# Optimization experiments

Measured on AMD Instinct MI355X. Metric: run time of the kernel, lower is better.

## Reference

```python
import jax, jax.numpy as jnp
import numpy as np

C1 = 0.01 ** 2
C2 = 0.03 ** 2
IN_CH = 3
WIN = 11
LEVELS = 5


def _gauss_kernel(k=WIN, sigma=1.5, c=IN_CH):
    ax = np.arange(k, dtype=np.float32) - (k - 1) / 2.0
    g = np.exp(-(ax ** 2) / (2.0 * sigma ** 2))
    g = g / g.sum()
    w2d = np.outer(g, g).astype(np.float32)  # [k,k]
    return jnp.asarray(np.tile(w2d[None, None], (c, 1, 1, 1)))  # [C,1,k,k]


def _dwconv(x, w):
    # depthwise (grouped) conv, 'same' padding for odd kernel
    pad = (w.shape[-1] - 1) // 2
    return jax.lax.conv_general_dilated(
        x, w, window_strides=(1, 1), padding=[(pad, pad), (pad, pad)],
        feature_group_count=x.shape[1],
        dimension_numbers=("NCHW", "OIHW", "NCHW"))


def _ssim_loss(i1, i2, w):
    m1 = _dwconv(i1, w)
    m2 = _dwconv(i2, w)
    m1sq = m1 * m1
    m2sq = m2 * m2
    m12 = m1 * m2
    s1 = _dwconv(i1 * i1, w) - m1sq
    s2 = _dwconv(i2 * i2, w) - m2sq
    s12 = _dwconv(i1 * i2, w) - m12
    ssim = (2 * m12 + C1) * (2 * s12 + C2) / ((m1sq + m2sq + C1) * (s1 + s2 + C2))
    return 1.0 - ssim.mean()


def _avg_pool2(x):
    B, C, H, W = x.shape
    return x.reshape(B, C, H // 2, 2, W // 2, 2).mean(axis=(3, 5))


def setup_inputs() -> dict:
    key = jax.random.key(0)
    k1, k2 = jax.random.split(key)
    img1 = jax.random.uniform(k1, (16, IN_CH, 512, 512), dtype=jnp.float32)
    img2 = jax.random.uniform(k2, (16, IN_CH, 512, 512), dtype=jnp.float32)
    inp = {"img1": img1, "img2": img2}
    for i in range(LEVELS):
        inp[f"g{i}"] = _gauss_kernel()
    return inp


def reference(img1, img2, g0, g1, g2, g3, g4):
    loss = jnp.asarray(0.0, dtype=img1.dtype)
    for w in (g0, g1, g2, g3, g4):
        loss = loss + _ssim_loss(img1, img2, w)
        img1 = _avg_pool2(img1)
        img2 = _avg_pool2(img2)
    return loss
```

## Files before the change

### kernel.cpp

```cpp
#include <hip/hip_runtime.h>
#include <math.h>

#define WIN 11
#define PAD 5
#define TW 64
#define TH 64

struct GW { float g[WIN]; };

template<bool EMIT>
__device__ __forceinline__ float ssim_wave_tile(
    const float* __restrict__ p1, const float* __restrict__ p2,
    int W, int X0, int Y0, const GW& gw, float2* __restrict__ rb,
    float* __restrict__ o1a, float* __restrict__ o1b, int Wout)
{
    const int lane = threadIdx.x & 63;
    const int gx = X0 + lane;
    const bool cval = gx < W;
    const int hx   = (lane < 5) ? (X0 - 5 + lane) : (X0 + 59 + lane);
    const bool hval = (lane < 10) && ((unsigned)hx < (unsigned)W);
    const int hpos = (lane < 5) ? lane : (64 + lane);
    const int cpos = 5 + lane;

    float vMp[11], vSp[11], vMq[11], vSq[11];
#pragma unroll
    for (int k = 0; k < 11; ++k) { vMp[k] = 0.f; vSp[k] = 0.f; vMq[k] = 0.f; vSq[k] = 0.f; }

    float part = 0.f;
    float pprev = 0.f, qprev = 0.f;
    float a, b, ah, bh;

    auto LOAD = [&](int t, float& oa, float& ob, float& oah, float& obh) {
        int y = Y0 - PAD + t;
        oa = 0.f; ob = 0.f; oah = 0.f; obh = 0.f;
        if ((unsigned)y < (unsigned)W) {
            const float* r1 = p1 + (size_t)y * W;
            const float* r2 = p2 + (size_t)y * W;
            if (cval) { oa  = r1[gx]; ob  = r2[gx]; }
            if (hval) { oah = r1[hx]; obh = r2[hx]; }
        }
    };

    LOAD(0, a, b, ah, bh);

#pragma unroll 2
    for (int t = 0; t < 74; ++t) {
        float na, nb, nah, nbh;
        LOAD(t + 1, na, nb, nah, nbh);

        float p = a + b, q = a - b;
        float ph = ah + bh, qh = ah - bh;
        rb[cpos] = make_float2(p, q);
        if (lane < 10) rb[hpos] = make_float2(ph, qh);
        __builtin_amdgcn_wave_barrier();

        float hp = 0.f, hq = 0.f, hpp = 0.f, hqq = 0.f;
#pragma unroll
        for (int j = 0; j < WIN; ++j) {
            float2 v = rb[lane + j];
            float g = gw.g[j];
            hp  = fmaf(g, v.x, hp);
            hpp = fmaf(g, v.x * v.x, hpp);
            hq  = fmaf(g, v.y, hq);
            hqq = fmaf(g, v.y * v.y, hqq);
        }
        __builtin_amdgcn_wave_barrier();

#pragma unroll
        for (int k = 0; k < 11; ++k) {
            float g = gw.g[10 - k];
            vMp[k] = fmaf(g, hp,  vMp[k]);
            vSp[k] = fmaf(g, hpp, vSp[k]);
            vMq[k] = fmaf(g, hq,  vMq[k]);
            vSq[k] = fmaf(g, hqq, vSq[k]);
        }

        if (EMIT) {
            if (t >= 6 && t <= 68 && (t & 1) == 0) {
                float sp_ = p + pprev, sq_ = q + qprev;
                float sp2 = sp_ + __shfl_down(sp_, 1, 64);
                float sq2 = sq_ + __shfl_down(sq_, 1, 64);
                if ((lane & 1) == 0) {
                    float P = sp2 * 0.25f, Q = sq2 * 0.25f;
                    int yo = (t - 6) >> 1;
                    size_t oo = (size_t)((Y0 >> 1) + yo) * Wout + ((X0 >> 1) + (lane >> 1));
                    o1a[oo] = (P + Q) * 0.5f;
                    o1b[oo] = (P - Q) * 0.5f;
                }
            }
            pprev = p; qprev = q;
        }

        if (t >= 10) {
            int o = t - 10;
            bool yok = (unsigned)(Y0 + o) < (unsigned)W;
            float Mp = vMp[0], Sp_ = vSp[0], Mq = vMq[0], Sq_ = vSq[0];
            const float C1v = 1e-4f, C2v = 9e-4f;
            float A = Mp * Mp, B = Mq * Mq;
            float ABp = A + B, ABm = A - B;
            float SSp = Sp_ + Sq_, SSm = Sp_ - Sq_;
            float n1 = fmaf(0.5f, ABm, C1v);
            float n2 = fmaf(0.5f, SSm - ABm, C2v);
            float e1 = fmaf(0.5f, ABp, C1v);
            float e2 = fmaf(0.5f, SSp - ABp, C2v);
            float v = (n1 * n2) * __builtin_amdgcn_rcpf(e1 * e2);
            part += (cval && yok) ? v : 0.f;
        }

#pragma unroll
        for (int k = 0; k < 10; ++k) {
            vMp[k] = vMp[k + 1]; vSp[k] = vSp[k + 1];
            vMq[k] = vMq[k + 1]; vSq[k] = vSq[k + 1];
        }
        vMp[10] = 0.f; vSp[10] = 0.f; vMq[10] = 0.f; vSq[10] = 0.f;

        a = na; b = nb; ah = nah; bh = nbh;
    }

    return part;
}

__global__ __launch_bounds__(256, 4) void ssim_l0_kernel(
    const float* __restrict__ i1, const float* __restrict__ i2,
    float* __restrict__ a1, float* __restrict__ b1,
    double* __restrict__ acc, GW gw)
{
    __shared__ float2 rbs[4][80];
    const int wid = threadIdx.x >> 6;
    const int w = blockIdx.x * 4 + wid;
    const int img = w >> 6;
    const int tt = w & 63;
    const int tx = tt & 7, ty = tt >> 3;
    const size_t off  = (size_t)img * 512 * 512;
    const size_t ooff = (size_t)img * 256 * 256;

    float part = ssim_wave_tile<true>(i1 + off, i2 + off, 512, tx * TW, ty * TH,
                                      gw, rbs[wid], a1 + ooff, b1 + ooff, 256);
#pragma unroll
    for (int o = 32; o > 0; o >>= 1) part += __shfl_down(part, o, 64);
    if ((threadIdx.x & 63) == 0) atomicAdd(acc, (double)part);
}

__global__ __launch_bounds__(256, 4) void ssim_rest_kernel(
    const float* __restrict__ a1, const float* __restrict__ b1,
    const float* __restrict__ a2, const float* __restrict__ b2,
    const float* __restrict__ a3, const float* __restrict__ b3,
    const float* __restrict__ a4, const float* __restrict__ b4,
    double* __restrict__ acc, GW gw)
{
    __shared__ float2 rbs[4][80];
    const int wid = threadIdx.x >> 6;
    const int w = blockIdx.x * 4 + wid;
    const int img = w / 22;
    const int r = w - img * 22;
    int lvl, tx, ty;
    if (r < 16)      { lvl = 1; tx = r & 3;        ty = r >> 2; }
    else if (r < 20) { lvl = 2; tx = (r - 16) & 1; ty = (r - 16) >> 1; }
    else if (r == 20){ lvl = 3; tx = 0; ty = 0; }
    else             { lvl = 4; tx = 0; ty = 0; }
    const int W = 512 >> lvl;
    const float* p1; const float* p2;
    switch (lvl) {
      case 1:  p1 = a1; p2 = b1; break;
      case 2:  p1 = a2; p2 = b2; break;
      case 3:  p1 = a3; p2 = b3; break;
      default: p1 = a4; p2 = b4; break;
    }
    const size_t off = (size_t)img * W * W;

    float part = ssim_wave_tile<false>(p1 + off, p2 + off, W, tx * TW, ty * TH,
                                       gw, rbs[wid], nullptr, nullptr, 0);
#pragma unroll
    for (int o = 32; o > 0; o >>= 1) part += __shfl_down(part, o, 64);
    if ((threadIdx.x & 63) == 0) atomicAdd(acc + lvl, (double)part);
}

__global__ __launch_bounds__(256) void pool_rest_kernel(
    const float* __restrict__ a1, const float* __restrict__ b1,
    float* __restrict__ a2, float* __restrict__ b2,
    float* __restrict__ a3, float* __restrict__ b3,
    float* __restrict__ a4, float* __restrict__ b4)
{
    __shared__ float l2[32][33];
    __shared__ float l3[16][17];
    const int tid = threadIdx.x;
    const int im = blockIdx.y;
    const int tb = blockIdx.x;
    const int tx = tb & 3, ty = tb >> 2;
    const bool second = im >= 48;
    const int ii = second ? im - 48 : im;
    const float* src = (second ? b1 : a1) + (size_t)ii * 256 * 256;
    float* o2 = (second ? b2 : a2) + (size_t)ii * 128 * 128;
    float* o3 = (second ? b3 : a3) + (size_t)ii * 64 * 64;
    float* o4 = (second ? b4 : a4) + (size_t)ii * 32 * 32;
    const int X0 = tx * 64, Y0 = ty * 64;

#pragma unroll
    for (int k = 0; k < 2; ++k) {
        int idx = tid + k * 256;
        int xp = idx & 15;
        int yo = idx >> 4;
        const float* rp = src + (size_t)(Y0 + 2 * yo) * 256 + (X0 + 4 * xp);
        float4 r0 = *(const float4*)rp;
        float4 r1 = *(const float4*)(rp + 256);
        float v0 = (r0.x + r0.y + r1.x + r1.y) * 0.25f;
        float v1 = (r0.z + r0.w + r1.z + r1.w) * 0.25f;
        l2[yo][2 * xp]     = v0;
        l2[yo][2 * xp + 1] = v1;
        float2* op = (float2*)(o2 + (size_t)((Y0 >> 1) + yo) * 128 + ((X0 >> 1) + 2 * xp));
        *op = make_float2(v0, v1);
    }
    __syncthreads();
    {
        int xo = tid & 15, yo = tid >> 4;
        if (yo < 16) {
            float v = (l2[2*yo][2*xo] + l2[2*yo][2*xo+1] +
                       l2[2*yo+1][2*xo] + l2[2*yo+1][2*xo+1]) * 0.25f;
            l3[yo][xo] = v;
            o3[(size_t)((Y0 >> 2) + yo) * 64 + ((X0 >> 2) + xo)] = v;
        }
    }
    __syncthreads();
    if (tid < 64) {
        int xo = tid & 7, yo = tid >> 3;
        float v = (l3[2*yo][2*xo] + l3[2*yo][2*xo+1] +
                   l3[2*yo+1][2*xo] + l3[2*yo+1][2*xo+1]) * 0.25f;
        o4[(size_t)((Y0 >> 3) + yo) * 32 + ((X0 >> 3) + xo)] = v;
    }
}

__global__ void final_kernel(const double* __restrict__ acc, float* __restrict__ out)
{
    double loss = 0.0;
#pragma unroll
    for (int l = 0; l < 5; ++l) {
        double cnt = 48.0 * (double)(512 >> l) * (double)(512 >> l);
        loss += 1.0 - acc[l] / cnt;
    }
    out[0] = (float)loss;
}

extern "C" void kernel_launch(void* const* d_in, const int* in_sizes, int n_in,
                              void* d_out, int out_size, void* d_ws, size_t ws_size,
                              hipStream_t stream)
{
    const float* img1 = (const float*)d_in[0];
    const float* img2 = (const float*)d_in[1];
    float* out = (float*)d_out;

    GW gw;
    double gs[WIN], sum = 0.0;
    for (int i = 0; i < WIN; ++i) {
        double ax = (double)i - 5.0;
        gs[i] = exp(-(ax * ax) / 4.5);
        sum += gs[i];
    }
    for (int i = 0; i < WIN; ++i) gw.g[i] = (float)(gs[i] / sum);

    double* acc = (double*)d_ws;
    float* base = (float*)((char*)d_ws + 64);
    const size_t n1 = 48ull * 256 * 256;
    const size_t n2 = 48ull * 128 * 128;
    const size_t n3 = 48ull * 64 * 64;
    const size_t n4 = 48ull * 32 * 32;
    float* a1 = base;      float* b1 = a1 + n1;
    float* a2 = b1 + n1;   float* b2 = a2 + n2;
    float* a3 = b2 + n2;   float* b3 = a3 + n3;
    float* a4 = b3 + n3;   float* b4 = a4 + n4;

    hipMemsetAsync(acc, 0, 5 * sizeof(double), stream);

    hipLaunchKernelGGL(ssim_l0_kernel, dim3(768), dim3(256), 0, stream,
                       img1, img2, a1, b1, acc, gw);

    hipLaunchKernelGGL(pool_rest_kernel, dim3(16, 96), dim3(256), 0, stream,
                       a1, b1, a2, b2, a3, b3, a4, b4);

    hipLaunchKernelGGL(ssim_rest_kernel, dim3(264), dim3(256), 0, stream,
                       a1, b1, a2, b2, a3, b3, a4, b4, acc, gw);

    hipLaunchKernelGGL(final_kernel, dim3(1), dim3(1), 0, stream, acc, out);
}
```

Before: 267.6 us.

## Fuse full pooling pyramid into level-0 SSIM kernel and halve tile height

The level-0 SSIM kernel now builds all pyramid levels 1-4 with cascaded wave shuffles, so the separate pool kernel and its global reread of level 1 are gone. Tile height drops from 64 to 32 rows, which doubles the wave count for both SSIM kernels and adds more halo rows per output row (42 loaded rows per 32 outputs instead of 74 per 64). Occupancy hint raised to 5 blocks per CU. The trade-off is more redundant halo loads and vertical convolution work plus extra shuffle and branch logic in the hot loop, in exchange for one fewer launch and better parallelism on the small levels.

```diff
diff --git a/kernel.cpp b/kernel.cpp
--- a/kernel.cpp
+++ b/kernel.cpp
@@ -4,15 +4,15 @@
 #define WIN 11
 #define PAD 5
 #define TW 64
-#define TH 64
 
 struct GW { float g[WIN]; };
-
-template<bool EMIT>
+struct Pyr { float *a1, *b1, *a2, *b2, *a3, *b3, *a4, *b4; };
+
+template<int TH_, bool EMIT>
 __device__ __forceinline__ float ssim_wave_tile(
     const float* __restrict__ p1, const float* __restrict__ p2,
     int W, int X0, int Y0, const GW& gw, float2* __restrict__ rb,
-    float* __restrict__ o1a, float* __restrict__ o1b, int Wout)
+    const Pyr* pyr)
 {
     const int lane = threadIdx.x & 63;
     const int gx = X0 + lane;
@@ -28,6 +28,9 @@
 
     float part = 0.f;
     float pprev = 0.f, qprev = 0.f;
+    float P1prev = 0.f, Q1prev = 0.f;
+    float P2prev = 0.f, Q2prev = 0.f;
+    float P3prev = 0.f, Q3prev = 0.f;
     float a, b, ah, bh;
 
     auto LOAD = [&](int t, float& oa, float& ob, float& oah, float& obh) {
@@ -44,7 +47,7 @@
     LOAD(0, a, b, ah, bh);
 
 #pragma unroll 2
-    for (int t = 0; t < 74; ++t) {
+    for (int t = 0; t < TH_ + 10; ++t) {
         float na, nb, nah, nbh;
         LOAD(t + 1, na, nb, nah, nbh);
 
@@ -76,17 +79,53 @@
         }
 
         if (EMIT) {
-            if (t >= 6 && t <= 68 && (t & 1) == 0) {
+            if (t >= 6 && t <= TH_ + 4 && (t & 1) == 0) {
                 float sp_ = p + pprev, sq_ = q + qprev;
                 float sp2 = sp_ + __shfl_down(sp_, 1, 64);
                 float sq2 = sq_ + __shfl_down(sq_, 1, 64);
+                float P1 = sp2 * 0.25f, Q1 = sq2 * 0.25f;
+                int yo = (t - 6) >> 1;
                 if ((lane & 1) == 0) {
-                    float P = sp2 * 0.25f, Q = sq2 * 0.25f;
-                    int yo = (t - 6) >> 1;
-                    size_t oo = (size_t)((Y0 >> 1) + yo) * Wout + ((X0 >> 1) + (lane >> 1));
-                    o1a[oo] = (P + Q) * 0.5f;
-                    o1b[oo] = (P - Q) * 0.5f;
+                    size_t oo = (size_t)((Y0 >> 1) + yo) * 256 + ((X0 >> 1) + (lane >> 1));
+                    pyr->a1[oo] = (P1 + Q1) * 0.5f;
+                    pyr->b1[oo] = (P1 - Q1) * 0.5f;
                 }
+                if (yo & 1) {
+                    float s2p = P1prev + P1, s2q = Q1prev + Q1;
+                    s2p += __shfl_down(s2p, 2, 64);
+                    s2q += __shfl_down(s2q, 2, 64);
+                    float P2 = s2p * 0.25f, Q2 = s2q * 0.25f;
+                    int zo = yo >> 1;
+                    if ((lane & 3) == 0) {
+                        size_t oo = (size_t)((Y0 >> 2) + zo) * 128 + ((X0 >> 2) + (lane >> 2));
+                        pyr->a2[oo] = (P2 + Q2) * 0.5f;
+                        pyr->b2[oo] = (P2 - Q2) * 0.5f;
+                    }
+                    if (zo & 1) {
+                        float s3p = P2prev + P2, s3q = Q2prev + Q2;
+                        s3p += __shfl_down(s3p, 4, 64);
+                        s3q += __shfl_down(s3q, 4, 64);
+                        float P3 = s3p * 0.25f, Q3 = s3q * 0.25f;
+                        int wo = zo >> 1;
+                        if ((lane & 7) == 0) {
+                            size_t oo = (size_t)((Y0 >> 3) + wo) * 64 + ((X0 >> 3) + (lane >> 3));
+                            pyr->a3[oo] = (P3 + Q3) * 0.5f;
+                            pyr->b3[oo] = (P3 - Q3) * 0.5f;
+                        }
+                        if (wo & 1) {
+                            float s4p = P3prev + P3, s4q = Q3prev + Q3;
+                            s4p += __shfl_down(s4p, 8, 64);
+                            s4q += __shfl_down(s4q, 8, 64);
+                            float P4 = s4p * 0.25f, Q4 = s4q * 0.25f;
+                            int uo = wo >> 1;
+                            if ((lane & 15) == 0) {
+                                size_t oo = (size_t)((Y0 >> 4) + uo) * 32 + ((X0 >> 4) + (lane >> 4));
+                                pyr->a4[oo] = (P4 + Q4) * 0.5f;
+                                pyr->b4[oo] = (P4 - Q4) * 0.5f;
+                            }
+                        } else { P3prev = P3; Q3prev = Q3; }
+                    } else { P2prev = P2; Q2prev = Q2; }
+                } else { P1prev = P1; Q1prev = Q1; }
             }
             pprev = p; qprev = q;
         }
@@ -120,22 +159,29 @@
     return part;
 }
 
-__global__ __launch_bounds__(256, 4) void ssim_l0_kernel(
+__global__ __launch_bounds__(256, 5) void ssim_l0_kernel(
     const float* __restrict__ i1, const float* __restrict__ i2,
     float* __restrict__ a1, float* __restrict__ b1,
+    float* __restrict__ a2, float* __restrict__ b2,
+    float* __restrict__ a3, float* __restrict__ b3,
+    float* __restrict__ a4, float* __restrict__ b4,
     double* __restrict__ acc, GW gw)
 {
     __shared__ float2 rbs[4][80];
     const int wid = threadIdx.x >> 6;
     const int w = blockIdx.x * 4 + wid;
-    const int img = w >> 6;
-    const int tt = w & 63;
+    const int img = w >> 7;
+    const int tt = w & 127;
     const int tx = tt & 7, ty = tt >> 3;
-    const size_t off  = (size_t)img * 512 * 512;
-    const size_t ooff = (size_t)img * 256 * 256;
-
-    float part = ssim_wave_tile<true>(i1 + off, i2 + off, 512, tx * TW, ty * TH,
-                                      gw, rbs[wid], a1 + ooff, b1 + ooff, 256);
+    const size_t off = (size_t)img * 512 * 512;
+    Pyr pyr;
+    pyr.a1 = a1 + (size_t)img * 256 * 256;  pyr.b1 = b1 + (size_t)img * 256 * 256;
+    pyr.a2 = a2 + (size_t)img * 128 * 128;  pyr.b2 = b2 + (size_t)img * 128 * 128;
+    pyr.a3 = a3 + (size_t)img * 64 * 64;    pyr.b3 = b3 + (size_t)img * 64 * 64;
+    pyr.a4 = a4 + (size_t)img * 32 * 32;    pyr.b4 = b4 + (size_t)img * 32 * 32;
+
+    float part = ssim_wave_tile<32, true>(i1 + off, i2 + off, 512,
+                                          tx * TW, ty * 32, gw, rbs[wid], &pyr);
 #pragma unroll
     for (int o = 32; o > 0; o >>= 1) part += __shfl_down(part, o, 64);
     if ((threadIdx.x & 63) == 0) atomicAdd(acc, (double)part);
@@ -151,12 +197,12 @@
     __shared__ float2 rbs[4][80];
     const int wid = threadIdx.x >> 6;
     const int w = blockIdx.x * 4 + wid;
-    const int img = w / 22;
-    const int r = w - img * 22;
+    const int img = w / 43;
+    const int r = w - img * 43;
     int lvl, tx, ty;
-    if (r < 16)      { lvl = 1; tx = r & 3;        ty = r >> 2; }
-    else if (r < 20) { lvl = 2; tx = (r - 16) & 1; ty = (r - 16) >> 1; }
-    else if (r == 20){ lvl = 3; tx = 0; ty = 0; }
+    if (r < 32)      { lvl = 1; tx = r & 3;        ty = r >> 2; }
+    else if (r < 40) { lvl = 2; tx = (r - 32) & 1; ty = (r - 32) >> 1; }
+    else if (r < 42) { lvl = 3; tx = 0; ty = r - 40; }
     else             { lvl = 4; tx = 0; ty = 0; }
     const int W = 512 >> lvl;
     const float* p1; const float* p2;
@@ -168,65 +214,11 @@
     }
     const size_t off = (size_t)img * W * W;
 
-    float part = ssim_wave_tile<false>(p1 + off, p2 + off, W, tx * TW, ty * TH,
-                                       gw, rbs[wid], nullptr, nullptr, 0);
+    float part = ssim_wave_tile<32, false>(p1 + off, p2 + off, W,
+                                           tx * TW, ty * 32, gw, rbs[wid], nullptr);
 #pragma unroll
     for (int o = 32; o > 0; o >>= 1) part += __shfl_down(part, o, 64);
     if ((threadIdx.x & 63) == 0) atomicAdd(acc + lvl, (double)part);
-}
-
-__global__ __launch_bounds__(256) void pool_rest_kernel(
-    const float* __restrict__ a1, const float* __restrict__ b1,
-    float* __restrict__ a2, float* __restrict__ b2,
-    float* __restrict__ a3, float* __restrict__ b3,
-    float* __restrict__ a4, float* __restrict__ b4)
-{
-    __shared__ float l2[32][33];
-    __shared__ float l3[16][17];
-    const int tid = threadIdx.x;
-    const int im = blockIdx.y;
-    const int tb = blockIdx.x;
-    const int tx = tb & 3, ty = tb >> 2;
-    const bool second = im >= 48;
-    const int ii = second ? im - 48 : im;
-    const float* src = (second ? b1 : a1) + (size_t)ii * 256 * 256;
-    float* o2 = (second ? b2 : a2) + (size_t)ii * 128 * 128;
-    float* o3 = (second ? b3 : a3) + (size_t)ii * 64 * 64;
-    float* o4 = (second ? b4 : a4) + (size_t)ii * 32 * 32;
-    const int X0 = tx * 64, Y0 = ty * 64;
-
-#pragma unroll
-    for (int k = 0; k < 2; ++k) {
-        int idx = tid + k * 256;
-        int xp = idx & 15;
-        int yo = idx >> 4;
-        const float* rp = src + (size_t)(Y0 + 2 * yo) * 256 + (X0 + 4 * xp);
-        float4 r0 = *(const float4*)rp;
-        float4 r1 = *(const float4*)(rp + 256);
-        float v0 = (r0.x + r0.y + r1.x + r1.y) * 0.25f;
-        float v1 = (r0.z + r0.w + r1.z + r1.w) * 0.25f;
-        l2[yo][2 * xp]     = v0;
-        l2[yo][2 * xp + 1] = v1;
-        float2* op = (float2*)(o2 + (size_t)((Y0 >> 1) + yo) * 128 + ((X0 >> 1) + 2 * xp));
-        *op = make_float2(v0, v1);
-    }
-    __syncthreads();
-    {
-        int xo = tid & 15, yo = tid >> 4;
-        if (yo < 16) {
-            float v = (l2[2*yo][2*xo] + l2[2*yo][2*xo+1] +
-                       l2[2*yo+1][2*xo] + l2[2*yo+1][2*xo+1]) * 0.25f;
-            l3[yo][xo] = v;
-            o3[(size_t)((Y0 >> 2) + yo) * 64 + ((X0 >> 2) + xo)] = v;
-        }
-    }
-    __syncthreads();
-    if (tid < 64) {
-        int xo = tid & 7, yo = tid >> 3;
-        float v = (l3[2*yo][2*xo] + l3[2*yo][2*xo+1] +
-                   l3[2*yo+1][2*xo] + l3[2*yo+1][2*xo+1]) * 0.25f;
-        o4[(size_t)((Y0 >> 3) + yo) * 32 + ((X0 >> 3) + xo)] = v;
-    }
 }
 
 __global__ void final_kernel(const double* __restrict__ acc, float* __restrict__ out)
@@ -270,13 +262,10 @@
 
     hipMemsetAsync(acc, 0, 5 * sizeof(double), stream);
 
-    hipLaunchKernelGGL(ssim_l0_kernel, dim3(768), dim3(256), 0, stream,
-                       img1, img2, a1, b1, acc, gw);
-
-    hipLaunchKernelGGL(pool_rest_kernel, dim3(16, 96), dim3(256), 0, stream,
-                       a1, b1, a2, b2, a3, b3, a4, b4);
-
-    hipLaunchKernelGGL(ssim_rest_kernel, dim3(264), dim3(256), 0, stream,
+    hipLaunchKernelGGL(ssim_l0_kernel, dim3(1536), dim3(256), 0, stream,
+                       img1, img2, a1, b1, a2, b2, a3, b3, a4, b4, acc, gw);
+
+    hipLaunchKernelGGL(ssim_rest_kernel, dim3(516), dim3(256), 0, stream,
                        a1, b1, a2, b2, a3, b3, a4, b4, acc, gw);
 
     hipLaunchKernelGGL(final_kernel, dim3(1), dim3(1), 0, stream, acc, out);
```

Measured after the change: 490.0 us. 83.1% more time.
